# Performance work log

Measured on AMD Instinct MI355X. Metric: run time of the kernel, lower is better.

Reference implementation:

```python
import jax, jax.numpy as jnp
import numpy as np

B, X, S, D_IN, D_OUT = 8, 8, 1024, 512, 64


def setup_inputs() -> dict:
    key = jax.random.key(0)
    ks = jax.random.split(key, 6)
    return {
        "inputs_for_keys": jax.random.normal(ks[0], (B, X, S, D_IN), dtype=jnp.float32),
        "inputs_for_values": jax.random.normal(ks[1], (B, X, S, D_IN), dtype=jnp.float32),
        "inputs_for_queries": jax.random.normal(ks[2], (B, X, S, D_IN), dtype=jnp.float32),
        "k_weight": jax.random.normal(ks[3], (D_IN, D_OUT), dtype=jnp.float32) * (2.0 / (D_IN + D_OUT)) ** 0.5,
        "v_weight": jax.random.normal(ks[4], (D_IN, D_OUT), dtype=jnp.float32) * (2.0 / (D_IN + D_OUT)) ** 0.5,
        "q_weight": jax.random.normal(ks[5], (D_IN, D_OUT), dtype=jnp.float32) * (2.0 / (D_IN + D_OUT)) ** 0.5,
    }


def reference(inputs_for_keys, inputs_for_values, inputs_for_queries, k_weight, v_weight, q_weight):
    # Projections: 'ixjk,kl->ixjl'
    K = jnp.einsum('bxsk,kl->bxsl', inputs_for_keys, k_weight)
    V = jnp.einsum('bxsk,kl->bxsl', inputs_for_values, v_weight)
    Q = jnp.einsum('bxsk,kl->bxsl', inputs_for_queries, q_weight)
    wk = K.shape[2]  # window_size_keys (NOTE: original scales by sqrt(seq_len), not sqrt(d_k))
    scores = jnp.einsum('bxqd,bxkd->bxqk', Q, K) / jnp.sqrt(jnp.float32(wk))
    # causal mask: triu(-inf, k=1) since is_self_attention=True
    causal = jnp.triu(jnp.ones((Q.shape[2], wk), dtype=bool), k=1)  # [Sq, Sk]
    scores = jnp.where(causal[None, None, :, :], -jnp.inf, scores)
    attn = jax.nn.softmax(scores, axis=-1)
    return jnp.einsum('bxqk,bxkd->bxqd', attn, V)
```

## Files before the change

### kernel.cpp

```cpp
#include <hip/hip_runtime.h>
#include <hip/hip_bf16.h>


typedef short  short8 __attribute__((ext_vector_type(8)));
typedef float  f32x4  __attribute__((ext_vector_type(4)));

#define DIN   512
#define DOUT  64
#define SEQ   1024
#define NROWS 65536

__device__ __forceinline__ unsigned short f2bf(float f) {
    unsigned int u = __float_as_uint(f);
    u += 0x7FFF + ((u >> 16) & 1);
    return (unsigned short)(u >> 16);
}

__device__ __forceinline__ unsigned short f2bf_rhu(float f) {
    return (unsigned short)((__float_as_uint(f) + 0x8000u) >> 16);
}

__device__ __forceinline__ float fast_exp2(float x) {
    float r;
    asm("v_exp_f32 %0, %1" : "=v"(r) : "v"(x));
    return r;
}

__global__ __launch_bounds__(256)
void wprep_kernel(const float* __restrict__ k_w, const float* __restrict__ v_w,
                  const float* __restrict__ q_w, unsigned short* __restrict__ Wfrag)
{
    const int mode = blockIdx.y;
    const float* w = (mode == 0) ? k_w : (mode == 1) ? v_w : q_w;
    const float sc = (mode == 2) ? 0.0450842200277801f : 1.0f;
    unsigned short* outp = Wfrag + (size_t)mode * 32768;

    const int s  = blockIdx.x * 256 + threadIdx.x;
    const int l  = s & 63;
    const int nt = (s >> 6) & 3;
    const int kk = s >> 8;
    const int lr = l & 15, lg = l >> 4;
    short8 frag;
    #pragma unroll
    for (int j = 0; j < 8; ++j)
        frag[j] = (short)f2bf(w[(kk * 32 + lg * 8 + j) * 64 + nt * 16 + lr] * sc);
    *(short8*)&outp[(size_t)s * 8] = frag;
}

__global__ __launch_bounds__(512, 2)
void proj_kernel(const float* __restrict__ k_in, const float* __restrict__ v_in,
                 const float* __restrict__ q_in,
                 const unsigned short* __restrict__ Wfrag,
                 unsigned short* __restrict__ Kb, unsigned short* __restrict__ Vf,
                 unsigned short* __restrict__ Qb)
{
    const int mode = blockIdx.y;
    const float* in = (mode == 0) ? k_in : (mode == 1) ? v_in : q_in;
    const unsigned short* wf = Wfrag + (size_t)mode * 32768;

    __shared__ __align__(16) unsigned short Wlds[32768];
    __shared__ __align__(16) unsigned short Alds[8][2][2048];

    const int tid = threadIdx.x;
    const int wid = tid >> 6;
    const int l   = tid & 63;
    const int lr  = l & 15;
    const int lg  = l >> 4;
    const int r0  = blockIdx.x * 128 + wid * 16;

    const int srow = l >> 5;
    const int scolb = (l & 31) * 8;
    const float* sbase = in + (size_t)(r0 + srow) * DIN + (l & 31) * 4;

    f32x4 rA[8], rB[8];

    #define LOADC(r, c)                                                        \
        { _Pragma("unroll")                                                    \
          for (int i = 0; i < 8; ++i)                                          \
              r[i] = __builtin_nontemporal_load(                               \
                  (const f32x4*)(sbase + (size_t)(2 * i) * DIN + (c) * 128)); }

    #define WRITEC(buf, r)                                                     \
        { _Pragma("unroll")                                                    \
          for (int i = 0; i < 8; ++i) {                                        \
              const int row = 2 * i + srow;                                    \
              ushort4 pk;                                                      \
              pk.x = f2bf(r[i].x); pk.y = f2bf(r[i].y);                        \
              pk.z = f2bf(r[i].z); pk.w = f2bf(r[i].w);                        \
              *(ushort4*)((char*)&Alds[wid][buf][0] +                          \
                  ((row * 256 + scolb) ^ ((row & 7) << 4))) = pk;              \
          } }

    const int abase = lr * 256 + lg * 16;
    const int aswz  = (lr & 7) << 4;

    f32x4 acc[4];
    #pragma unroll
    for (int nt = 0; nt < 4; ++nt)
        #pragma unroll
        for (int i = 0; i < 4; ++i) acc[nt][i] = 0.f;

    #define COMPUTEC(buf, c)                                                   \
        { _Pragma("unroll")                                                    \
          for (int k = 0; k < 4; ++k) {                                        \
              const short8 af = *(const short8*)((const char*)&Alds[wid][buf][0] + \
                                  ((abase + k * 64) ^ aswz));                  \
              const int kk = (c) * 4 + k;                                      \
              _Pragma("unroll")                                                \
              for (int nt = 0; nt < 4; ++nt) {                                 \
                  const short8 bf = *(const short8*)&Wlds[((kk * 4 + nt) * 64 + l) * 8]; \
                  acc[nt] = __builtin_amdgcn_mfma_f32_16x16x32_bf16(af, bf, acc[nt], 0, 0, 0); \
              }                                                                \
          } }

    LOADC(rA, 0);
    LOADC(rB, 1);
    #pragma unroll
    for (int i = 0; i < 8; ++i)
        *(short8*)&Wlds[(i * 512 + tid) * 8] = *(const short8*)&wf[(size_t)(i * 512 + tid) * 8];
    __syncthreads();

    WRITEC(0, rA);
    LOADC(rA, 2);
    COMPUTEC(0, 0);

    WRITEC(1, rB);
    LOADC(rB, 3);
    COMPUTEC(1, 1);

    WRITEC(0, rA);
    COMPUTEC(0, 2);

    WRITEC(1, rB);
    COMPUTEC(1, 3);

    if (mode == 1) {
        const int grow = r0 + lg * 4;
        const int bx = grow >> 10;
        const int sl = grow & 1023;
        const int sg = sl >> 5;
        const int lp = (((sl & 31) >> 3) << 4) | lr;
        const int j0 = sl & 7;
        #pragma unroll
        for (int nt = 0; nt < 4; ++nt) {
            ushort4 pk;
            pk.x = f2bf(acc[nt][0]); pk.y = f2bf(acc[nt][1]);
            pk.z = f2bf(acc[nt][2]); pk.w = f2bf(acc[nt][3]);
            *(ushort4*)&Vf[(((size_t)bx * 32 + sg) * 4 + nt) * 512 + (size_t)lp * 8 + j0] = pk;
        }
    } else {
        unsigned short* outp = (mode == 0) ? Kb : Qb;
        const int rbase = r0 + lg * 4;
        #pragma unroll
        for (int nt = 0; nt < 4; ++nt)
            #pragma unroll
            for (int i = 0; i < 4; ++i)
                outp[(size_t)(rbase + i) * 64 + nt * 16 + lr] = f2bf(acc[nt][i]);
    }
    #undef LOADC
    #undef WRITEC
    #undef COMPUTEC
}

__global__ __launch_bounds__(512)
void attn_kernel(const unsigned short* __restrict__ Qb,
                 const unsigned short* __restrict__ Kb,
                 const unsigned short* __restrict__ Vf,
                 float* __restrict__ out)
{
    __shared__ __align__(16) unsigned short Plds[8][16][72];
    __shared__ __align__(16) f32x4 RedAcc[4][64][4];
    __shared__ float RedSum[4][64][4];

    const int tid  = threadIdx.x;
    const int wid  = tid >> 6;
    const int g    = wid & 3;
    const int half = wid >> 2;
    const int l    = tid & 63;
    const int lr   = l & 15;
    const int lg   = l >> 4;
    const int bx   = blockIdx.x;
    const int qblk = 15 - (int)blockIdx.y;
    const int qw0  = qblk * 64 + g * 16;

    const unsigned short* Qp = Qb + (size_t)bx * 65536;
    const unsigned short* Kp = Kb + (size_t)bx * 65536;
    const unsigned short* Vp = Vf + (size_t)bx * 65536;

    const short8 qa0 = *(const short8*)&Qp[(size_t)(qw0 + lr) * 64 + lg * 8];
    const short8 qa1 = *(const short8*)&Qp[(size_t)(qw0 + lr) * 64 + 32 + lg * 8];

    const int qrow = qw0 + lg * 4;

    float lsum[4] = {0.f, 0.f, 0.f, 0.f};
    f32x4 acc[4];
    #pragma unroll
    for (int dt = 0; dt < 4; ++dt)
        #pragma unroll
        for (int i = 0; i < 4; ++i) acc[dt][i] = 0.f;

    for (int kb = half * 64; kb <= qw0; kb += 128) {
        #pragma unroll
        for (int kt = 0; kt < 4; ++kt) {
            const int kbase = kb + kt * 16;
            if (kbase <= qw0) {
                const short8 k0 = *(const short8*)&Kp[(size_t)(kbase + lr) * 64 + lg * 8];
                const short8 k1 = *(const short8*)&Kp[(size_t)(kbase + lr) * 64 + 32 + lg * 8];
                f32x4 t;
                #pragma unroll
                for (int i = 0; i < 4; ++i) t[i] = 0.f;
                t = __builtin_amdgcn_mfma_f32_16x16x32_bf16(qa0, k0, t, 0, 0, 0);
                t = __builtin_amdgcn_mfma_f32_16x16x32_bf16(qa1, k1, t, 0, 0, 0);
                const int kcol = kbase + lr;
                #pragma unroll
                for (int i = 0; i < 4; ++i) {
                    const float p = (kcol <= qrow + i) ? fast_exp2(t[i] - 8.0f) : 0.f;
                    lsum[i] += p;
                    Plds[wid][lg * 4 + i][kt * 16 + lr] = f2bf_rhu(p);
                }
            } else {
                #pragma unroll
                for (int i = 0; i < 4; ++i)
                    Plds[wid][lg * 4 + i][kt * 16 + lr] = 0;
            }
        }

        asm volatile("s_waitcnt lgkmcnt(0)" ::: "memory");
        __builtin_amdgcn_sched_barrier(0);

        #pragma unroll
        for (int c = 0; c < 2; ++c) {
            if (kb + c * 32 <= qw0 + 15) {
                const short8 pa = *(const short8*)&Plds[wid][lr][c * 32 + lg * 8];
                const size_t vbase = ((size_t)((kb >> 5) + c) * 4) * 512;
                #pragma unroll
                for (int dt = 0; dt < 4; ++dt) {
                    const short8 vbd = *(const short8*)
                        &Vp[vbase + (size_t)dt * 512 + (size_t)l * 8];
                    acc[dt] = __builtin_amdgcn_mfma_f32_16x16x32_bf16(pa, vbd, acc[dt], 0, 0, 0);
                }
            }
        }
        asm volatile("s_waitcnt lgkmcnt(0)" ::: "memory");
    }

    if (half == 1) {
        #pragma unroll
        for (int dt = 0; dt < 4; ++dt) RedAcc[g][l][dt] = acc[dt];
        #pragma unroll
        for (int i = 0; i < 4; ++i) RedSum[g][l][i] = lsum[i];
    }
    __syncthreads();
    if (half == 0) {
        #pragma unroll
        for (int dt = 0; dt < 4; ++dt) acc[dt] += RedAcc[g][l][dt];
        #pragma unroll
        for (int i = 0; i < 4; ++i) lsum[i] += RedSum[g][l][i];

        #pragma unroll
        for (int d = 1; d < 16; d <<= 1)
            #pragma unroll
            for (int i = 0; i < 4; ++i) lsum[i] += __shfl_xor(lsum[i], d);

        float inv[4];
        #pragma unroll
        for (int i = 0; i < 4; ++i) inv[i] = 1.0f / lsum[i];

        const size_t orow = (size_t)bx * 1024 + qw0;
        #pragma unroll
        for (int dt = 0; dt < 4; ++dt)
            #pragma unroll
            for (int i = 0; i < 4; ++i)
                out[(orow + lg * 4 + i) * 64 + dt * 16 + lr] = acc[dt][i] * inv[i];
    }
}

extern "C" void kernel_launch(void* const* d_in, const int* in_sizes, int n_in,
                              void* d_out, int out_size, void* d_ws, size_t ws_size,
                              hipStream_t stream) {
    const float* k_in = (const float*)d_in[0];
    const float* v_in = (const float*)d_in[1];
    const float* q_in = (const float*)d_in[2];
    const float* k_w  = (const float*)d_in[3];
    const float* v_w  = (const float*)d_in[4];
    const float* q_w  = (const float*)d_in[5];

    unsigned short* Kb    = (unsigned short*)d_ws;
    unsigned short* Vf    = Kb + (size_t)NROWS * 64;
    unsigned short* Qb    = Vf + (size_t)NROWS * 64;
    unsigned short* Wfrag = Qb + (size_t)NROWS * 64;

    wprep_kernel<<<dim3(16, 3), 256, 0, stream>>>(k_w, v_w, q_w, Wfrag);
    proj_kernel<<<dim3(512, 3), 512, 0, stream>>>(
        k_in, v_in, q_in, Wfrag, Kb, Vf, Qb);
    attn_kernel<<<dim3(64, 16), 512, 0, stream>>>(Qb, Kb, Vf, (float*)d_out);
}
```

Baseline: 128.5 us.

## Process two query tiles per attention block to reuse K and V loads

Each attention block now handles 128 query rows (two 64-row tiles, q0 and q0+64) instead of 64. Each loaded K fragment and V fragment feeds MFMAs for both tiles, halving global K/V traffic per query. The grid shrinks from 64x16 to 64x8 blocks. Register pressure and LDS use roughly double, which may lower occupancy, and fewer, less uniform blocks are launched.

```diff
diff --git a/kernel.cpp b/kernel.cpp
--- a/kernel.cpp
+++ b/kernel.cpp
@@ -168,9 +168,9 @@
                  const unsigned short* __restrict__ Vf,
                  float* __restrict__ out)
 {
-    __shared__ __align__(16) unsigned short Plds[8][16][72];
-    __shared__ __align__(16) f32x4 RedAcc[4][64][4];
-    __shared__ float RedSum[4][64][4];
+    __shared__ __align__(16) unsigned short Plds[8][2][16][72];
+    __shared__ __align__(16) f32x4 RedAcc[4][2][64][4];
+    __shared__ float RedSum[4][2][64][4];
 
     const int tid  = threadIdx.x;
     const int wid  = tid >> 6;
@@ -180,48 +180,72 @@
     const int lr   = l & 15;
     const int lg   = l >> 4;
     const int bx   = blockIdx.x;
-    const int qblk = 15 - (int)blockIdx.y;
-    const int qw0  = qblk * 64 + g * 16;
+    const int qs   = 7 - (int)blockIdx.y;
+    const int q0   = qs * 128 + g * 16;
+    const int q1   = q0 + 64;
 
     const unsigned short* Qp = Qb + (size_t)bx * 65536;
     const unsigned short* Kp = Kb + (size_t)bx * 65536;
     const unsigned short* Vp = Vf + (size_t)bx * 65536;
 
-    const short8 qa0 = *(const short8*)&Qp[(size_t)(qw0 + lr) * 64 + lg * 8];
-    const short8 qa1 = *(const short8*)&Qp[(size_t)(qw0 + lr) * 64 + 32 + lg * 8];
-
-    const int qrow = qw0 + lg * 4;
-
-    float lsum[4] = {0.f, 0.f, 0.f, 0.f};
-    f32x4 acc[4];
+    const short8 qa0 = *(const short8*)&Qp[(size_t)(q0 + lr) * 64 + lg * 8];
+    const short8 qa1 = *(const short8*)&Qp[(size_t)(q0 + lr) * 64 + 32 + lg * 8];
+    const short8 qb0 = *(const short8*)&Qp[(size_t)(q1 + lr) * 64 + lg * 8];
+    const short8 qb1 = *(const short8*)&Qp[(size_t)(q1 + lr) * 64 + 32 + lg * 8];
+
+    const int qrow0 = q0 + lg * 4;
+    const int qrow1 = q1 + lg * 4;
+
+    float lsum0[4] = {0.f, 0.f, 0.f, 0.f};
+    float lsum1[4] = {0.f, 0.f, 0.f, 0.f};
+    f32x4 acc0[4], acc1[4];
     #pragma unroll
     for (int dt = 0; dt < 4; ++dt)
         #pragma unroll
-        for (int i = 0; i < 4; ++i) acc[dt][i] = 0.f;
-
-    for (int kb = half * 64; kb <= qw0; kb += 128) {
+        for (int i = 0; i < 4; ++i) { acc0[dt][i] = 0.f; acc1[dt][i] = 0.f; }
+
+    for (int kb = half * 64; kb <= q1; kb += 128) {
         #pragma unroll
         for (int kt = 0; kt < 4; ++kt) {
             const int kbase = kb + kt * 16;
-            if (kbase <= qw0) {
+            if (kbase <= q1) {
                 const short8 k0 = *(const short8*)&Kp[(size_t)(kbase + lr) * 64 + lg * 8];
                 const short8 k1 = *(const short8*)&Kp[(size_t)(kbase + lr) * 64 + 32 + lg * 8];
                 f32x4 t;
                 #pragma unroll
                 for (int i = 0; i < 4; ++i) t[i] = 0.f;
-                t = __builtin_amdgcn_mfma_f32_16x16x32_bf16(qa0, k0, t, 0, 0, 0);
-                t = __builtin_amdgcn_mfma_f32_16x16x32_bf16(qa1, k1, t, 0, 0, 0);
+                t = __builtin_amdgcn_mfma_f32_16x16x32_bf16(qb0, k0, t, 0, 0, 0);
+                t = __builtin_amdgcn_mfma_f32_16x16x32_bf16(qb1, k1, t, 0, 0, 0);
                 const int kcol = kbase + lr;
                 #pragma unroll
                 for (int i = 0; i < 4; ++i) {
-                    const float p = (kcol <= qrow + i) ? fast_exp2(t[i] - 8.0f) : 0.f;
-                    lsum[i] += p;
-                    Plds[wid][lg * 4 + i][kt * 16 + lr] = f2bf_rhu(p);
+                    const float p = (kcol <= qrow1 + i) ? fast_exp2(t[i] - 8.0f) : 0.f;
+                    lsum1[i] += p;
+                    Plds[wid][1][lg * 4 + i][kt * 16 + lr] = f2bf_rhu(p);
+                }
+                if (kbase <= q0) {
+                    f32x4 u;
+                    #pragma unroll
+                    for (int i = 0; i < 4; ++i) u[i] = 0.f;
+                    u = __builtin_amdgcn_mfma_f32_16x16x32_bf16(qa0, k0, u, 0, 0, 0);
+                    u = __builtin_amdgcn_mfma_f32_16x16x32_bf16(qa1, k1, u, 0, 0, 0);
+                    #pragma unroll
+                    for (int i = 0; i < 4; ++i) {
+                        const float p = (kcol <= qrow0 + i) ? fast_exp2(u[i] - 8.0f) : 0.f;
+                        lsum0[i] += p;
+                        Plds[wid][0][lg * 4 + i][kt * 16 + lr] = f2bf_rhu(p);
+                    }
+                } else {
+                    #pragma unroll
+                    for (int i = 0; i < 4; ++i)
+                        Plds[wid][0][lg * 4 + i][kt * 16 + lr] = 0;
                 }
             } else {
                 #pragma unroll
-                for (int i = 0; i < 4; ++i)
-                    Plds[wid][lg * 4 + i][kt * 16 + lr] = 0;
+                for (int i = 0; i < 4; ++i) {
+                    Plds[wid][0][lg * 4 + i][kt * 16 + lr] = 0;
+                    Plds[wid][1][lg * 4 + i][kt * 16 + lr] = 0;
+                }
             }
         }
 
@@ -230,14 +254,21 @@
 
         #pragma unroll
         for (int c = 0; c < 2; ++c) {
-            if (kb + c * 32 <= qw0 + 15) {
-                const short8 pa = *(const short8*)&Plds[wid][lr][c * 32 + lg * 8];
+            if (kb + c * 32 <= q1 + 15) {
                 const size_t vbase = ((size_t)((kb >> 5) + c) * 4) * 512;
-                #pragma unroll
-                for (int dt = 0; dt < 4; ++dt) {
-                    const short8 vbd = *(const short8*)
-                        &Vp[vbase + (size_t)dt * 512 + (size_t)l * 8];
-                    acc[dt] = __builtin_amdgcn_mfma_f32_16x16x32_bf16(pa, vbd, acc[dt], 0, 0, 0);
+                short8 vv[4];
+                #pragma unroll
+                for (int dt = 0; dt < 4; ++dt)
+                    vv[dt] = *(const short8*)&Vp[vbase + (size_t)dt * 512 + (size_t)l * 8];
+                const short8 pa1 = *(const short8*)&Plds[wid][1][lr][c * 32 + lg * 8];
+                #pragma unroll
+                for (int dt = 0; dt < 4; ++dt)
+                    acc1[dt] = __builtin_amdgcn_mfma_f32_16x16x32_bf16(pa1, vv[dt], acc1[dt], 0, 0, 0);
+                if (kb + c * 32 <= q0 + 15) {
+                    const short8 pa0 = *(const short8*)&Plds[wid][0][lr][c * 32 + lg * 8];
+                    #pragma unroll
+                    for (int dt = 0; dt < 4; ++dt)
+                        acc0[dt] = __builtin_amdgcn_mfma_f32_16x16x32_bf16(pa0, vv[dt], acc0[dt], 0, 0, 0);
                 }
             }
         }
@@ -246,32 +277,53 @@
 
     if (half == 1) {
         #pragma unroll
-        for (int dt = 0; dt < 4; ++dt) RedAcc[g][l][dt] = acc[dt];
-        #pragma unroll
-        for (int i = 0; i < 4; ++i) RedSum[g][l][i] = lsum[i];
+        for (int dt = 0; dt < 4; ++dt) {
+            RedAcc[g][0][l][dt] = acc0[dt];
+            RedAcc[g][1][l][dt] = acc1[dt];
+        }
+        #pragma unroll
+        for (int i = 0; i < 4; ++i) {
+            RedSum[g][0][l][i] = lsum0[i];
+            RedSum[g][1][l][i] = lsum1[i];
+        }
     }
     __syncthreads();
     if (half == 0) {
         #pragma unroll
-        for (int dt = 0; dt < 4; ++dt) acc[dt] += RedAcc[g][l][dt];
-        #pragma unroll
-        for (int i = 0; i < 4; ++i) lsum[i] += RedSum[g][l][i];
+        for (int dt = 0; dt < 4; ++dt) {
+            acc0[dt] += RedAcc[g][0][l][dt];
+            acc1[dt] += RedAcc[g][1][l][dt];
+        }
+        #pragma unroll
+        for (int i = 0; i < 4; ++i) {
+            lsum0[i] += RedSum[g][0][l][i];
+            lsum1[i] += RedSum[g][1][l][i];
+        }
 
         #pragma unroll
         for (int d = 1; d < 16; d <<= 1)
             #pragma unroll
-            for (int i = 0; i < 4; ++i) lsum[i] += __shfl_xor(lsum[i], d);
-
-        float inv[4];
-        #pragma unroll
-        for (int i = 0; i < 4; ++i) inv[i] = 1.0f / lsum[i];
-
-        const size_t orow = (size_t)bx * 1024 + qw0;
+            for (int i = 0; i < 4; ++i) {
+                lsum0[i] += __shfl_xor(lsum0[i], d);
+                lsum1[i] += __shfl_xor(lsum1[i], d);
+            }
+
+        float inv0[4], inv1[4];
+        #pragma unroll
+        for (int i = 0; i < 4; ++i) {
+            inv0[i] = 1.0f / lsum0[i];
+            inv1[i] = 1.0f / lsum1[i];
+        }
+
+        const size_t orow0 = (size_t)bx * 1024 + q0;
+        const size_t orow1 = (size_t)bx * 1024 + q1;
         #pragma unroll
         for (int dt = 0; dt < 4; ++dt)
             #pragma unroll
-            for (int i = 0; i < 4; ++i)
-                out[(orow + lg * 4 + i) * 64 + dt * 16 + lr] = acc[dt][i] * inv[i];
+            for (int i = 0; i < 4; ++i) {
+                out[(orow0 + lg * 4 + i) * 64 + dt * 16 + lr] = acc0[dt][i] * inv0[i];
+                out[(orow1 + lg * 4 + i) * 64 + dt * 16 + lr] = acc1[dt][i] * inv1[i];
+            }
     }
 }
 
@@ -293,5 +345,5 @@
     wprep_kernel<<<dim3(16, 3), 256, 0, stream>>>(k_w, v_w, q_w, Wfrag);
     proj_kernel<<<dim3(512, 3), 512, 0, stream>>>(
         k_in, v_in, q_in, Wfrag, Kb, Vf, Qb);
-    attn_kernel<<<dim3(64, 16), 512, 0, stream>>>(Qb, Kb, Vf, (float*)d_out);
-}
+    attn_kernel<<<dim3(64, 8), 512, 0, stream>>>(Qb, Kb, Vf, (float*)d_out);
+}
```

Measured after the change: 117.4 us. 1.1x faster.

## Process four query tiles per attention block to reuse K/V loads

Applied to the files above, without the earlier changes.

Each attention block now covers four strided 64-row query tiles instead of one, so each wave keeps four Q fragments in registers. Every K and V fragment it loads is reused across up to four query tiles, and the grid shrinks from 16 to 4 blocks in y. This cuts global and L2 traffic for K/V. In exchange it uses far more registers and LDS per block (roughly 64 accumulator floats per lane plus a 4x larger P buffer), the launch bounds now ask for 2 blocks per CU, and there are fewer blocks in total (256), which may hurt occupancy and load balance across CUs.

```diff
diff --git a/kernel.cpp b/kernel.cpp
--- a/kernel.cpp
+++ b/kernel.cpp
@@ -162,15 +162,15 @@
     #undef COMPUTEC
 }
 
-__global__ __launch_bounds__(512)
+__global__ __launch_bounds__(512, 2)
 void attn_kernel(const unsigned short* __restrict__ Qb,
                  const unsigned short* __restrict__ Kb,
                  const unsigned short* __restrict__ Vf,
                  float* __restrict__ out)
 {
-    __shared__ __align__(16) unsigned short Plds[8][16][72];
-    __shared__ __align__(16) f32x4 RedAcc[4][64][4];
-    __shared__ float RedSum[4][64][4];
+    __shared__ __align__(16) unsigned short Plds[8][4][16][72];
+    __shared__ __align__(16) f32x4 RedAcc[4][4][64][4];
+    __shared__ float RedSum[4][4][64][4];
 
     const int tid  = threadIdx.x;
     const int wid  = tid >> 6;
@@ -180,48 +180,69 @@
     const int lr   = l & 15;
     const int lg   = l >> 4;
     const int bx   = blockIdx.x;
-    const int qblk = 15 - (int)blockIdx.y;
-    const int qw0  = qblk * 64 + g * 16;
+    const int qs   = 3 - (int)blockIdx.y;
+    const int q0   = qs * 256 + g * 16;
 
     const unsigned short* Qp = Qb + (size_t)bx * 65536;
     const unsigned short* Kp = Kb + (size_t)bx * 65536;
     const unsigned short* Vp = Vf + (size_t)bx * 65536;
 
-    const short8 qa0 = *(const short8*)&Qp[(size_t)(qw0 + lr) * 64 + lg * 8];
-    const short8 qa1 = *(const short8*)&Qp[(size_t)(qw0 + lr) * 64 + 32 + lg * 8];
-
-    const int qrow = qw0 + lg * 4;
-
-    float lsum[4] = {0.f, 0.f, 0.f, 0.f};
-    f32x4 acc[4];
-    #pragma unroll
-    for (int dt = 0; dt < 4; ++dt)
-        #pragma unroll
-        for (int i = 0; i < 4; ++i) acc[dt][i] = 0.f;
-
-    for (int kb = half * 64; kb <= qw0; kb += 128) {
+    short8 qa[4][2];
+    #pragma unroll
+    for (int tt = 0; tt < 4; ++tt) {
+        qa[tt][0] = *(const short8*)&Qp[(size_t)(q0 + tt * 64 + lr) * 64 + lg * 8];
+        qa[tt][1] = *(const short8*)&Qp[(size_t)(q0 + tt * 64 + lr) * 64 + 32 + lg * 8];
+    }
+
+    float lsum[4][4];
+    f32x4 acc[4][4];
+    #pragma unroll
+    for (int tt = 0; tt < 4; ++tt)
+        #pragma unroll
+        for (int dt = 0; dt < 4; ++dt) {
+            #pragma unroll
+            for (int i = 0; i < 4; ++i) acc[tt][dt][i] = 0.f;
+            lsum[tt][dt] = 0.f;
+        }
+
+    const int q3 = q0 + 192;
+
+    for (int kb = half * 64; kb <= q3; kb += 128) {
         #pragma unroll
         for (int kt = 0; kt < 4; ++kt) {
             const int kbase = kb + kt * 16;
-            if (kbase <= qw0) {
+            if (kbase <= q3) {
                 const short8 k0 = *(const short8*)&Kp[(size_t)(kbase + lr) * 64 + lg * 8];
                 const short8 k1 = *(const short8*)&Kp[(size_t)(kbase + lr) * 64 + 32 + lg * 8];
-                f32x4 t;
-                #pragma unroll
-                for (int i = 0; i < 4; ++i) t[i] = 0.f;
-                t = __builtin_amdgcn_mfma_f32_16x16x32_bf16(qa0, k0, t, 0, 0, 0);
-                t = __builtin_amdgcn_mfma_f32_16x16x32_bf16(qa1, k1, t, 0, 0, 0);
                 const int kcol = kbase + lr;
                 #pragma unroll
-                for (int i = 0; i < 4; ++i) {
-                    const float p = (kcol <= qrow + i) ? fast_exp2(t[i] - 8.0f) : 0.f;
-                    lsum[i] += p;
-                    Plds[wid][lg * 4 + i][kt * 16 + lr] = f2bf_rhu(p);
+                for (int tt = 0; tt < 4; ++tt) {
+                    const int qt = q0 + tt * 64;
+                    if (kbase <= qt) {
+                        f32x4 t;
+                        #pragma unroll
+                        for (int i = 0; i < 4; ++i) t[i] = 0.f;
+                        t = __builtin_amdgcn_mfma_f32_16x16x32_bf16(qa[tt][0], k0, t, 0, 0, 0);
+                        t = __builtin_amdgcn_mfma_f32_16x16x32_bf16(qa[tt][1], k1, t, 0, 0, 0);
+                        const int qrow = qt + lg * 4;
+                        #pragma unroll
+                        for (int i = 0; i < 4; ++i) {
+                            const float p = (kcol <= qrow + i) ? fast_exp2(t[i] - 8.0f) : 0.f;
+                            lsum[tt][i] += p;
+                            Plds[wid][tt][lg * 4 + i][kt * 16 + lr] = f2bf_rhu(p);
+                        }
+                    } else {
+                        #pragma unroll
+                        for (int i = 0; i < 4; ++i)
+                            Plds[wid][tt][lg * 4 + i][kt * 16 + lr] = 0;
+                    }
                 }
             } else {
                 #pragma unroll
-                for (int i = 0; i < 4; ++i)
-                    Plds[wid][lg * 4 + i][kt * 16 + lr] = 0;
+                for (int tt = 0; tt < 4; ++tt)
+                    #pragma unroll
+                    for (int i = 0; i < 4; ++i)
+                        Plds[wid][tt][lg * 4 + i][kt * 16 + lr] = 0;
             }
         }
 
@@ -230,14 +251,21 @@
 
         #pragma unroll
         for (int c = 0; c < 2; ++c) {
-            if (kb + c * 32 <= qw0 + 15) {
-                const short8 pa = *(const short8*)&Plds[wid][lr][c * 32 + lg * 8];
+            if (kb + c * 32 <= q3 + 15) {
                 const size_t vbase = ((size_t)((kb >> 5) + c) * 4) * 512;
-                #pragma unroll
-                for (int dt = 0; dt < 4; ++dt) {
-                    const short8 vbd = *(const short8*)
-                        &Vp[vbase + (size_t)dt * 512 + (size_t)l * 8];
-                    acc[dt] = __builtin_amdgcn_mfma_f32_16x16x32_bf16(pa, vbd, acc[dt], 0, 0, 0);
+                short8 vv[4];
+                #pragma unroll
+                for (int dt = 0; dt < 4; ++dt)
+                    vv[dt] = *(const short8*)&Vp[vbase + (size_t)dt * 512 + (size_t)l * 8];
+                #pragma unroll
+                for (int tt = 0; tt < 4; ++tt) {
+                    if (kb + c * 32 <= q0 + tt * 64 + 15) {
+                        const short8 pa = *(const short8*)&Plds[wid][tt][lr][c * 32 + lg * 8];
+                        #pragma unroll
+                        for (int dt = 0; dt < 4; ++dt)
+                            acc[tt][dt] = __builtin_amdgcn_mfma_f32_16x16x32_bf16(
+                                pa, vv[dt], acc[tt][dt], 0, 0, 0);
+                    }
                 }
             }
         }
@@ -246,32 +274,43 @@
 
     if (half == 1) {
         #pragma unroll
-        for (int dt = 0; dt < 4; ++dt) RedAcc[g][l][dt] = acc[dt];
-        #pragma unroll
-        for (int i = 0; i < 4; ++i) RedSum[g][l][i] = lsum[i];
+        for (int tt = 0; tt < 4; ++tt) {
+            #pragma unroll
+            for (int dt = 0; dt < 4; ++dt) RedAcc[g][tt][l][dt] = acc[tt][dt];
+            #pragma unroll
+            for (int i = 0; i < 4; ++i) RedSum[g][tt][l][i] = lsum[tt][i];
+        }
     }
     __syncthreads();
     if (half == 0) {
         #pragma unroll
-        for (int dt = 0; dt < 4; ++dt) acc[dt] += RedAcc[g][l][dt];
-        #pragma unroll
-        for (int i = 0; i < 4; ++i) lsum[i] += RedSum[g][l][i];
+        for (int tt = 0; tt < 4; ++tt) {
+            #pragma unroll
+            for (int dt = 0; dt < 4; ++dt) acc[tt][dt] += RedAcc[g][tt][l][dt];
+            #pragma unroll
+            for (int i = 0; i < 4; ++i) lsum[tt][i] += RedSum[g][tt][l][i];
+        }
 
         #pragma unroll
         for (int d = 1; d < 16; d <<= 1)
             #pragma unroll
-            for (int i = 0; i < 4; ++i) lsum[i] += __shfl_xor(lsum[i], d);
-
-        float inv[4];
-        #pragma unroll
-        for (int i = 0; i < 4; ++i) inv[i] = 1.0f / lsum[i];
-
-        const size_t orow = (size_t)bx * 1024 + qw0;
-        #pragma unroll
-        for (int dt = 0; dt < 4; ++dt)
-            #pragma unroll
-            for (int i = 0; i < 4; ++i)
-                out[(orow + lg * 4 + i) * 64 + dt * 16 + lr] = acc[dt][i] * inv[i];
+            for (int tt = 0; tt < 4; ++tt)
+                #pragma unroll
+                for (int i = 0; i < 4; ++i)
+                    lsum[tt][i] += __shfl_xor(lsum[tt][i], d);
+
+        #pragma unroll
+        for (int tt = 0; tt < 4; ++tt) {
+            float inv[4];
+            #pragma unroll
+            for (int i = 0; i < 4; ++i) inv[i] = 1.0f / lsum[tt][i];
+            const size_t orow = (size_t)bx * 1024 + q0 + tt * 64;
+            #pragma unroll
+            for (int dt = 0; dt < 4; ++dt)
+                #pragma unroll
+                for (int i = 0; i < 4; ++i)
+                    out[(orow + lg * 4 + i) * 64 + dt * 16 + lr] = acc[tt][dt][i] * inv[i];
+        }
     }
 }
 
@@ -293,5 +332,5 @@
     wprep_kernel<<<dim3(16, 3), 256, 0, stream>>>(k_w, v_w, q_w, Wfrag);
     proj_kernel<<<dim3(512, 3), 512, 0, stream>>>(
         k_in, v_in, q_in, Wfrag, Kb, Vf, Qb);
-    attn_kernel<<<dim3(64, 16), 512, 0, stream>>>(Qb, Kb, Vf, (float*)d_out);
-}
+    attn_kernel<<<dim3(64, 4), 512, 0, stream>>>(Qb, Kb, Vf, (float*)d_out);
+}
```

Result: faster. 125.1 us (-2.7%).
